# Kernel tuning notes

Measured on AMD Instinct MI355X. Metric: run time of the kernel, lower is better.

Reference implementation:

```python
import jax, jax.numpy as jnp
import numpy as np

N_NODES = 50000
N_EDGES = 800000
N_GRAPHS = 256
IN_DIM = 128
HID = 512            # hidden_layer_size
H2 = HID // 2        # 256, conv channels
H4 = HID // 4        # 128


def _linear_init(key, fan_in, fan_out):
    kw, kb = jax.random.split(key)
    bound = 1.0 / np.sqrt(fan_in)
    W = jax.random.uniform(kw, (fan_in, fan_out), minval=-bound, maxval=bound, dtype=jnp.float32)
    b = jax.random.uniform(kb, (fan_out,), minval=-bound, maxval=bound, dtype=jnp.float32)
    return W, b


def setup_inputs() -> dict:
    key = jax.random.key(0)
    ks = jax.random.split(key, 8)
    x = jax.random.normal(ks[0], (N_NODES, IN_DIM), dtype=jnp.float32)
    edge_index = jax.random.randint(ks[1], (2, N_EDGES), 0, N_NODES, dtype=jnp.int64)
    batch = jnp.sort(jax.random.randint(ks[2], (N_NODES,), 0, N_GRAPHS, dtype=jnp.int64))
    W1, b1 = _linear_init(ks[3], IN_DIM, HID)
    Wc1, bc1 = _linear_init(ks[4], HID, H2)
    Wc2, bc2 = _linear_init(ks[5], H2, H2)
    W2, b2 = _linear_init(ks[6], H2, H4)
    W3, b3 = _linear_init(ks[7], H4, 1)
    return {"x": x, "edge_index": edge_index, "batch": batch,
            "W1": W1, "b1": b1, "Wc1": Wc1, "bc1": bc1,
            "Wc2": Wc2, "bc2": bc2, "W2": W2, "b2": b2, "W3": W3, "b3": b3}


def _gcn_conv(h, W, b, src, dst, norm):
    # PyG GCNConv: out = scatter_add(norm * (h @ W)[src] -> dst) + b
    hw = h @ W                                   # [N, C_out]
    msg = norm[:, None] * hw[src]                # [E+N, C_out] gather
    agg = jax.ops.segment_sum(msg, dst, num_segments=N_NODES)  # scatter-add
    return agg + b


def reference(x, edge_index, batch, W1, b1, Wc1, bc1, Wc2, bc2, W2, b2, W3, b3):
    # --- symmetric GCN normalization with self-loops (shared by both convs) ---
    loop = jnp.arange(N_NODES, dtype=edge_index.dtype)
    src = jnp.concatenate([edge_index[0], loop])
    dst = jnp.concatenate([edge_index[1], loop])
    deg = jax.ops.segment_sum(jnp.ones_like(dst, dtype=jnp.float32), dst, num_segments=N_NODES)
    dinv = jax.lax.rsqrt(deg)                    # deg >= 1 thanks to self-loops
    norm = dinv[src] * dinv[dst]                 # [E+N]

    h = jax.nn.relu(x @ W1 + b1)                 # lin1
    h = jax.nn.relu(_gcn_conv(h, Wc1, bc1, src, dst, norm))   # conv1
    h = jax.nn.relu(_gcn_conv(h, Wc2, bc2, src, dst, norm))   # conv2

    # global_mean_pool over graph ids
    sums = jax.ops.segment_sum(h, batch, num_segments=N_GRAPHS)
    counts = jax.ops.segment_sum(jnp.ones((N_NODES,), jnp.float32), batch, num_segments=N_GRAPHS)
    g = sums / jnp.maximum(counts, 1.0)[:, None]

    # F.dropout is identity in deterministic/eval reference
    g = jax.nn.relu(g @ W2 + b2)                 # lin2
    return g @ W3 + b3                           # lin3 -> [N_GRAPHS, 1]
```

## Files before the change

### kernel.cpp

```cpp
#include <hip/hip_runtime.h>
#include <hip/hip_bf16.h>

#define NN 50000
#define NE 800000
#define NG 256
#define DIN 128
#define DH 512
#define DC 256
#define DL 128
#define NSB 196

#define XBF_OFF   0UL
#define H1BF_OFF  12800000UL
#define HWBF_OFF  64000000UL
#define H2BF_OFF  89600000UL
#define H3BF_OFF  115200000UL
#define W1T_OFF   140800000UL
#define WC1T_OFF  140931072UL
#define WC2T_OFF  141193216UL
#define CNT_OFF   141324288UL
#define FILL_OFF  141524288UL
#define DINV_OFF  141724288UL
#define RP_OFF    141924288UL
#define BSUM_OFF  142124416UL
#define EW_OFF    142125440UL

using bf16x8 = __attribute__((ext_vector_type(8))) short;
using f32x4  = __attribute__((ext_vector_type(4))) float;

__device__ __forceinline__ short f2bf(float f) {
  unsigned u = __builtin_bit_cast(unsigned, f);
  unsigned r = u + 0x7fffu + ((u >> 16) & 1u);
  return (short)(r >> 16);
}
__device__ __forceinline__ float bf2f(unsigned short u) {
  return __builtin_bit_cast(float, (unsigned)u << 16);
}

__device__ __forceinline__ void gload_lds16(const void* g, void* l) {
  typedef const __attribute__((address_space(1))) unsigned gu32;
  typedef __attribute__((address_space(3))) unsigned lu32;
  __builtin_amdgcn_global_load_lds((gu32*)g, (lu32*)l, 16, 0, 0);
}

__global__ __launch_bounds__(256) void prep0(
    const int* __restrict__ src, const int* __restrict__ dst, int* __restrict__ cnt,
    const float* __restrict__ x, short* __restrict__ xbf,
    const float* __restrict__ W1, short* __restrict__ W1t,
    const float* __restrict__ Wc1, short* __restrict__ Wc1t,
    const float* __restrict__ Wc2, short* __restrict__ Wc2t) {
  long gidx = (long)blockIdx.x * 256 + threadIdx.x;
  if (gidx < NE) {
    atomicAdd(&cnt[dst[gidx]], 1);
    return;
  }
  long idx = gidx - NE;
  if (idx < 800000) {
    const float4* p = (const float4*)x + idx * 2;
    float4 a = p[0], b = p[1];
    bf16x8 o;
    o[0] = f2bf(a.x); o[1] = f2bf(a.y); o[2] = f2bf(a.z); o[3] = f2bf(a.w);
    o[4] = f2bf(b.x); o[5] = f2bf(b.y); o[6] = f2bf(b.z); o[7] = f2bf(b.w);
    *(bf16x8*)(xbf + idx * 8) = o;
  } else if (idx < 865536) {
    int j = (int)(idx - 800000);
    int n = j >> 7, k = j & 127;
    W1t[j] = f2bf(W1[k * DH + n]);
  } else if (idx < 996608) {
    int j = (int)(idx - 865536);
    int n = j >> 9, k = j & 511;
    Wc1t[j] = f2bf(Wc1[k * DC + n]);
  } else if (idx < 1062144) {
    int j = (int)(idx - 996608);
    int n = j >> 8, k = j & 255;
    Wc2t[j] = f2bf(Wc2[k * DC + n]);
  }
}

__device__ __forceinline__ void scan_p1_body(
    const int* __restrict__ cnt, int* __restrict__ rowptr,
    int* __restrict__ bsum, float* __restrict__ dinv) {
  __shared__ int wsum[4];
  const int b = blockIdx.x;
  const int idx = b * 256 + threadIdx.x;
  const int lane = threadIdx.x & 63, wid = threadIdx.x >> 6;
  int v = (idx < NN) ? cnt[idx] : 0;
  int incl = v;
  #pragma unroll
  for (int s = 1; s < 64; s <<= 1) {
    int t = __shfl_up(incl, s, 64);
    if (lane >= s) incl += t;
  }
  if (lane == 63) wsum[wid] = incl;
  __syncthreads();
  int woff = 0;
  for (int w = 0; w < wid; ++w) woff += wsum[w];
  if (idx < NN) {
    rowptr[idx] = woff + incl - v;
    dinv[idx] = 1.0f / sqrtf((float)(v + 1));
  }
  if (threadIdx.x == 255) bsum[b] = woff + incl;
}

__device__ __forceinline__ void scan_p3_body(
    int* __restrict__ rowptr, const int* __restrict__ bsum) {
  __shared__ int r4[4];
  const int b = blockIdx.x;
  const int t = threadIdx.x;
  const int lane = t & 63, wid = t >> 6;
  int v = (t < b) ? bsum[t] : 0;
  #pragma unroll
  for (int s = 32; s > 0; s >>= 1) v += __shfl_down(v, s, 64);
  if (lane == 0) r4[wid] = v;
  __syncthreads();
  const int off = r4[0] + r4[1] + r4[2] + r4[3];
  const int idx = b * 256 + t;
  if (idx < NN) rowptr[idx] += off;
  if (b == 0 && t == 0) rowptr[NN] = NE;
}

__global__ void fill_csr(const int* __restrict__ src, const int* __restrict__ dst,
                         const int* __restrict__ rowptr, int* __restrict__ fill,
                         const float* __restrict__ dinv, unsigned* __restrict__ ewp) {
  int e = blockIdx.x * blockDim.x + threadIdx.x;
  if (e < NE) {
    int d = dst[e];
    int s = src[e];
    int pos = rowptr[d] + atomicAdd(&fill[d], 1);
    float w = dinv[d] * dinv[s];
    ewp[pos] = (unsigned)s | ((unsigned)(unsigned short)f2bf(w) << 16);
  }
}

template<int DO_RELU, int HAS_BIAS>
__device__ __forceinline__ void gemm_body(
    const short* __restrict__ A, const short* __restrict__ Bt,
    const float* __restrict__ bias, short* __restrict__ Cout,
    int M, int K, int N, int bxi, int byi)
{
  __shared__ __align__(16) short As[128][64];
  __shared__ __align__(16) short Bs[128][64];
  const int tid  = threadIdx.x;
  const int lane = tid & 63;
  const int wave = tid >> 6;
  const int wr   = wave >> 1;
  const int wc   = wave & 1;
  const int bm = byi * 128;
  const int bn = bxi * 128;

  const int srow = lane >> 3;
  const int scol = ((lane & 7) ^ srow) * 8;

  f32x4 acc[4][4];
  #pragma unroll
  for (int m = 0; m < 4; ++m)
    #pragma unroll
    for (int n = 0; n < 4; ++n)
      acc[m][n] = f32x4{0.f, 0.f, 0.f, 0.f};

  const int fr  = lane & 15;
  const int g4  = lane >> 4;
  const int frx = fr & 7;

  for (int k0 = 0; k0 < K; k0 += 64) {
    #pragma unroll
    for (int j = 0; j < 4; ++j) {
      const int r = wave * 32 + j * 8;
      gload_lds16(A  + (long)(bm + r + srow) * K + k0 + scol, &As[r][0]);
      gload_lds16(Bt + (long)(bn + r + srow) * K + k0 + scol, &Bs[r][0]);
    }
    __syncthreads();
    #pragma unroll
    for (int kk = 0; kk < 2; ++kk) {
      const int col = ((kk * 4 + g4) ^ frx) * 8;
      bf16x8 af[4], bfr[4];
      #pragma unroll
      for (int m = 0; m < 4; ++m)
        af[m] = *(const bf16x8*)&As[wr * 64 + m * 16 + fr][col];
      #pragma unroll
      for (int n = 0; n < 4; ++n)
        bfr[n] = *(const bf16x8*)&Bs[wc * 64 + n * 16 + fr][col];
      #pragma unroll
      for (int m = 0; m < 4; ++m)
        #pragma unroll
        for (int n = 0; n < 4; ++n)
          acc[m][n] = __builtin_amdgcn_mfma_f32_16x16x32_bf16(af[m], bfr[n], acc[m][n], 0, 0, 0);
    }
    __syncthreads();
  }

  const int cr4 = (lane >> 4) * 4;
  const int cc  = lane & 15;
  #pragma unroll
  for (int m = 0; m < 4; ++m) {
    #pragma unroll
    for (int r = 0; r < 4; ++r) {
      int gm = bm + wr * 64 + m * 16 + cr4 + r;
      if (gm >= M) continue;
      #pragma unroll
      for (int n = 0; n < 4; ++n) {
        int gn = bn + wc * 64 + n * 16 + cc;
        float v = acc[m][n][r];
        if (HAS_BIAS) v += bias[gn];
        if (DO_RELU) v = fmaxf(v, 0.f);
        Cout[(long)gm * N + gn] = f2bf(v);
      }
    }
  }
}

__global__ __launch_bounds__(256) void gemm_lin1(
    const short* __restrict__ A, const short* __restrict__ Bt,
    const float* __restrict__ bias, short* __restrict__ Cout,
    const int* __restrict__ cnt, int* __restrict__ rowptr,
    int* __restrict__ bsum, float* __restrict__ dinv)
{
  if (blockIdx.x < NSB) { scan_p1_body(cnt, rowptr, bsum, dinv); return; }
  int gb = blockIdx.x - NSB;
  gemm_body<1, 1>(A, Bt, bias, Cout, NN, DIN, DH, gb & 3, gb >> 2);
}

__global__ __launch_bounds__(256) void gemm_conv1(
    const short* __restrict__ A, const short* __restrict__ Bt,
    short* __restrict__ Cout, int* __restrict__ rowptr,
    const int* __restrict__ bsum)
{
  if (blockIdx.x < NSB) { scan_p3_body(rowptr, bsum); return; }
  int gb = blockIdx.x - NSB;
  gemm_body<0, 0>(A, Bt, nullptr, Cout, NN, DH, DC, gb & 1, gb >> 1);
}

__global__ __launch_bounds__(256) void gemm_conv2(
    const short* __restrict__ A, const short* __restrict__ Bt,
    short* __restrict__ Cout)
{
  gemm_body<0, 0>(A, Bt, nullptr, Cout, NN, DC, DC, blockIdx.x & 1, blockIdx.x >> 1);
}

__global__ __launch_bounds__(256) void aggregate_v6(
    const unsigned short* __restrict__ hw, const unsigned* __restrict__ ewp,
    const int* __restrict__ rowptr, const float* __restrict__ dinv,
    const float* __restrict__ bias, unsigned short* __restrict__ out)
{
  const int wid  = threadIdx.x >> 6;
  const int lane = threadIdx.x & 63;
  const int i = blockIdx.x * 4 + wid;
  if (i >= NN) return;
  const int c0 = lane * 4;
  const float di = dinv[i];

  ushort4 sv = *(const ushort4*)(hw + (long)i * DC + c0);
  const float dii = di * di;
  float acc0 = dii * bf2f(sv.x);
  float acc1 = dii * bf2f(sv.y);
  float acc2 = dii * bf2f(sv.z);
  float acc3 = dii * bf2f(sv.w);

  const int s0 = rowptr[i], s1 = rowptr[i + 1];
  int e = s0;
  for (; e + 8 <= s1; e += 8) {
    unsigned pk[8]; ushort4 vv[8];
    #pragma unroll
    for (int j = 0; j < 8; ++j) pk[j] = __builtin_nontemporal_load(ewp + e + j);
    #pragma unroll
    for (int j = 0; j < 8; ++j)
      vv[j] = *(const ushort4*)(hw + (long)(pk[j] & 0xffffu) * DC + c0);
    #pragma unroll
    for (int j = 0; j < 8; ++j) {
      float w = bf2f((unsigned short)(pk[j] >> 16));
      acc0 += w * bf2f(vv[j].x);
      acc1 += w * bf2f(vv[j].y);
      acc2 += w * bf2f(vv[j].z);
      acc3 += w * bf2f(vv[j].w);
    }
  }
  for (; e + 4 <= s1; e += 4) {
    unsigned pk[4]; ushort4 vv[4];
    #pragma unroll
    for (int j = 0; j < 4; ++j) pk[j] = __builtin_nontemporal_load(ewp + e + j);
    #pragma unroll
    for (int j = 0; j < 4; ++j)
      vv[j] = *(const ushort4*)(hw + (long)(pk[j] & 0xffffu) * DC + c0);
    #pragma unroll
    for (int j = 0; j < 4; ++j) {
      float w = bf2f((unsigned short)(pk[j] >> 16));
      acc0 += w * bf2f(vv[j].x);
      acc1 += w * bf2f(vv[j].y);
      acc2 += w * bf2f(vv[j].z);
      acc3 += w * bf2f(vv[j].w);
    }
  }
  for (; e < s1; ++e) {
    unsigned pk = __builtin_nontemporal_load(ewp + e);
    float w = bf2f((unsigned short)(pk >> 16));
    ushort4 v = *(const ushort4*)(hw + (long)(pk & 0xffffu) * DC + c0);
    acc0 += w * bf2f(v.x);
    acc1 += w * bf2f(v.y);
    acc2 += w * bf2f(v.z);
    acc3 += w * bf2f(v.w);
  }
  const float4 bv = *(const float4*)(bias + c0);
  ushort4 o;
  o.x = (unsigned short)f2bf(fmaxf(acc0 + bv.x, 0.f));
  o.y = (unsigned short)f2bf(fmaxf(acc1 + bv.y, 0.f));
  o.z = (unsigned short)f2bf(fmaxf(acc2 + bv.z, 0.f));
  o.w = (unsigned short)f2bf(fmaxf(acc3 + bv.w, 0.f));
  unsigned long long po = __builtin_bit_cast(unsigned long long, o);
  __builtin_nontemporal_store(po, (unsigned long long*)(out + (long)i * DC + c0));
}

__global__ __launch_bounds__(256) void pool_mlp_v3(
    const unsigned short* __restrict__ h, const int* __restrict__ batch,
    const float* __restrict__ W2, const float* __restrict__ b2,
    const float* __restrict__ W3, const float* __restrict__ b3,
    float* __restrict__ out)
{
  __shared__ float part[4][DC];
  __shared__ float gmean[DC];
  __shared__ float red[DL];
  const int g = blockIdx.x;
  const int t = threadIdx.x;
  const int wid = t >> 6;
  const int lane = t & 63;
  const int c0 = lane * 4;

  int lo = 0, hi = NN;
  while (lo < hi) { int mid = (lo + hi) >> 1; if (batch[mid] < g) lo = mid + 1; else hi = mid; }
  const int start = lo;
  hi = NN;
  while (lo < hi) { int mid = (lo + hi) >> 1; if (batch[mid] < g + 1) lo = mid + 1; else hi = mid; }
  const int end = lo;

  float4 a0 = {0.f, 0.f, 0.f, 0.f}, a1 = {0.f, 0.f, 0.f, 0.f};
  int i = start + wid;
  for (; i + 4 < end; i += 8) {
    ushort4 v0 = *(const ushort4*)(h + (long)i * DC + c0);
    ushort4 v1 = *(const ushort4*)(h + (long)(i + 4) * DC + c0);
    a0.x += bf2f(v0.x); a0.y += bf2f(v0.y); a0.z += bf2f(v0.z); a0.w += bf2f(v0.w);
    a1.x += bf2f(v1.x); a1.y += bf2f(v1.y); a1.z += bf2f(v1.z); a1.w += bf2f(v1.w);
  }
  if (i < end) {
    ushort4 v0 = *(const ushort4*)(h + (long)i * DC + c0);
    a0.x += bf2f(v0.x); a0.y += bf2f(v0.y); a0.z += bf2f(v0.z); a0.w += bf2f(v0.w);
  }
  a0.x += a1.x; a0.y += a1.y; a0.z += a1.z; a0.w += a1.w;
  *(float4*)&part[wid][c0] = a0;
  __syncthreads();
  if (wid == 0) {
    const float inv = 1.0f / fmaxf((float)(end - start), 1.f);
    float4 s0 = *(const float4*)&part[0][c0];
    float4 s1 = *(const float4*)&part[1][c0];
    float4 s2 = *(const float4*)&part[2][c0];
    float4 s3 = *(const float4*)&part[3][c0];
    float4 m;
    m.x = (s0.x + s1.x + s2.x + s3.x) * inv;
    m.y = (s0.y + s1.y + s2.y + s3.y) * inv;
    m.z = (s0.z + s1.z + s2.z + s3.z) * inv;
    m.w = (s0.w + s1.w + s2.w + s3.w) * inv;
    *(float4*)&gmean[c0] = m;
  }
  __syncthreads();
  if (t < DL) {
    float acc = b2[t];
    for (int k = 0; k < DC; ++k) acc = fmaf(gmean[k], W2[k * DL + t], acc);
    red[t] = fmaxf(acc, 0.f) * W3[t];
  }
  __syncthreads();
  for (int s2 = 64; s2 > 0; s2 >>= 1) {
    if (t < s2) red[t] += red[t + s2];
    __syncthreads();
  }
  if (t == 0) out[g] = red[0] + b3[0];
}

extern "C" void kernel_launch(void* const* d_in, const int* in_sizes, int n_in,
                              void* d_out, int out_size, void* d_ws, size_t ws_size,
                              hipStream_t stream) {
  const float* x    = (const float*)d_in[0];
  const int*   ei   = (const int*)d_in[1];
  const int*   bat  = (const int*)d_in[2];
  const float* W1   = (const float*)d_in[3];
  const float* b1   = (const float*)d_in[4];
  const float* Wc1  = (const float*)d_in[5];
  const float* bc1  = (const float*)d_in[6];
  const float* Wc2  = (const float*)d_in[7];
  const float* bc2  = (const float*)d_in[8];
  const float* W2   = (const float*)d_in[9];
  const float* b2   = (const float*)d_in[10];
  const float* W3   = (const float*)d_in[11];
  const float* b3   = (const float*)d_in[12];
  float* out = (float*)d_out;

  char* ws = (char*)d_ws;
  short* xbf    = (short*)(ws + XBF_OFF);
  short* h1bf   = (short*)(ws + H1BF_OFF);
  unsigned short* hwbf = (unsigned short*)(ws + HWBF_OFF);
  unsigned short* h2bf = (unsigned short*)(ws + H2BF_OFF);
  unsigned short* h3bf = (unsigned short*)(ws + H3BF_OFF);
  short* W1t    = (short*)(ws + W1T_OFF);
  short* Wc1t   = (short*)(ws + WC1T_OFF);
  short* Wc2t   = (short*)(ws + WC2T_OFF);
  int*   cnt    = (int*)  (ws + CNT_OFF);
  int*   fill   = (int*)  (ws + FILL_OFF);
  float* dinv   = (float*)(ws + DINV_OFF);
  int*   rowptr = (int*)  (ws + RP_OFF);
  int*   bsum   = (int*)  (ws + BSUM_OFF);
  unsigned* ewp = (unsigned*)(ws + EW_OFF);

  const int* srcE = ei;
  const int* dstE = ei + NE;

  hipMemsetAsync(cnt, 0, 2 * NN * sizeof(int), stream);

  prep0<<<(NE + 1062144 + 255) / 256, 256, 0, stream>>>(
      srcE, dstE, cnt, x, xbf, W1, W1t, Wc1, Wc1t, Wc2, Wc2t);

  gemm_lin1<<<NSB + 4 * 391, 256, 0, stream>>>(xbf, W1t, b1, h1bf,
                                               cnt, rowptr, bsum, dinv);
  gemm_conv1<<<NSB + 2 * 391, 256, 0, stream>>>(h1bf, Wc1t, (short*)hwbf,
                                                rowptr, bsum);
  fill_csr<<<(NE + 255) / 256, 256, 0, stream>>>(srcE, dstE, rowptr, fill, dinv, ewp);

  aggregate_v6<<<(NN + 3) / 4, 256, 0, stream>>>(hwbf, ewp, rowptr, dinv, bc1, h2bf);
  gemm_conv2<<<2 * 391, 256, 0, stream>>>((const short*)h2bf, Wc2t, (short*)hwbf);
  aggregate_v6<<<(NN + 3) / 4, 256, 0, stream>>>(hwbf, ewp, rowptr, dinv, bc2, h3bf);

  pool_mlp_v3<<<NG, 256, 0, stream>>>(h3bf, bat, W2, b2, W3, b3, out);
}
```

Baseline: 306.2 us.

## Pad CSR rows to multiples of eight and software-pipeline edge loads

Each node's CSR row is padded up to a multiple of 8 entries. The edge buffer is zeroed by an enlarged memset, so padding entries have weight zero and point at node 0. The aggregation kernel drops its 4-wide and scalar tail loops and prefetches the next 8 packed edge words while it gathers features for the current 8. This removes loop-tail divergence and hides edge-index load latency, at the cost of extra zero-weight gathers and a larger edge buffer plus memset.

```diff
diff --git a/kernel.cpp b/kernel.cpp
--- a/kernel.cpp
+++ b/kernel.cpp
@@ -20,10 +20,10 @@
 #define WC2T_OFF  141193216UL
 #define CNT_OFF   141324288UL
 #define FILL_OFF  141524288UL
-#define DINV_OFF  141724288UL
-#define RP_OFF    141924288UL
-#define BSUM_OFF  142124416UL
-#define EW_OFF    142125440UL
+#define EW_OFF    141724288UL
+#define DINV_OFF  146524288UL
+#define RP_OFF    146724288UL
+#define BSUM_OFF  146924544UL
 
 using bf16x8 = __attribute__((ext_vector_type(8))) short;
 using f32x4  = __attribute__((ext_vector_type(4))) float;
@@ -84,8 +84,9 @@
   const int b = blockIdx.x;
   const int idx = b * 256 + threadIdx.x;
   const int lane = threadIdx.x & 63, wid = threadIdx.x >> 6;
-  int v = (idx < NN) ? cnt[idx] : 0;
-  int incl = v;
+  int v  = (idx < NN) ? cnt[idx] : 0;
+  int vp = (idx < NN) ? ((v + 7) & ~7) : 0;
+  int incl = vp;
   #pragma unroll
   for (int s = 1; s < 64; s <<= 1) {
     int t = __shfl_up(incl, s, 64);
@@ -95,10 +96,8 @@
   __syncthreads();
   int woff = 0;
   for (int w = 0; w < wid; ++w) woff += wsum[w];
-  if (idx < NN) {
-    rowptr[idx] = woff + incl - v;
-    dinv[idx] = 1.0f / sqrtf((float)(v + 1));
-  }
+  if (idx <= NN) rowptr[idx] = woff + incl - vp;
+  if (idx < NN)  dinv[idx] = 1.0f / sqrtf((float)(v + 1));
   if (threadIdx.x == 255) bsum[b] = woff + incl;
 }
 
@@ -115,8 +114,7 @@
   __syncthreads();
   const int off = r4[0] + r4[1] + r4[2] + r4[3];
   const int idx = b * 256 + t;
-  if (idx < NN) rowptr[idx] += off;
-  if (b == 0 && t == 0) rowptr[NN] = NE;
+  if (idx <= NN) rowptr[idx] += off;
 }
 
 __global__ void fill_csr(const int* __restrict__ src, const int* __restrict__ dst,
@@ -237,7 +235,7 @@
   gemm_body<0, 0>(A, Bt, nullptr, Cout, NN, DC, DC, blockIdx.x & 1, blockIdx.x >> 1);
 }
 
-__global__ __launch_bounds__(256) void aggregate_v6(
+__global__ __launch_bounds__(256) void aggregate_v9(
     const unsigned short* __restrict__ hw, const unsigned* __restrict__ ewp,
     const int* __restrict__ rowptr, const float* __restrict__ dinv,
     const float* __restrict__ bias, unsigned short* __restrict__ out)
@@ -250,55 +248,45 @@
   const float di = dinv[i];
 
   ushort4 sv = *(const ushort4*)(hw + (long)i * DC + c0);
+  const int s0 = rowptr[i], s1 = rowptr[i + 1];
+
+  unsigned pkA[8];
+  if (s0 < s1) {
+    #pragma unroll
+    for (int j = 0; j < 8; ++j) pkA[j] = __builtin_nontemporal_load(ewp + s0 + j);
+  }
+
   const float dii = di * di;
   float acc0 = dii * bf2f(sv.x);
   float acc1 = dii * bf2f(sv.y);
   float acc2 = dii * bf2f(sv.z);
   float acc3 = dii * bf2f(sv.w);
 
-  const int s0 = rowptr[i], s1 = rowptr[i + 1];
-  int e = s0;
-  for (; e + 8 <= s1; e += 8) {
-    unsigned pk[8]; ushort4 vv[8];
-    #pragma unroll
-    for (int j = 0; j < 8; ++j) pk[j] = __builtin_nontemporal_load(ewp + e + j);
+  for (int e = s0; e < s1; e += 8) {
+    ushort4 vv[8];
     #pragma unroll
     for (int j = 0; j < 8; ++j)
-      vv[j] = *(const ushort4*)(hw + (long)(pk[j] & 0xffffu) * DC + c0);
+      vv[j] = *(const ushort4*)(hw + (long)(pkA[j] & 0xffffu) * DC + c0);
+    unsigned pkB[8];
+    if (e + 8 < s1) {
+      #pragma unroll
+      for (int j = 0; j < 8; ++j) pkB[j] = __builtin_nontemporal_load(ewp + e + 8 + j);
+    } else {
+      #pragma unroll
+      for (int j = 0; j < 8; ++j) pkB[j] = 0u;
+    }
     #pragma unroll
     for (int j = 0; j < 8; ++j) {
-      float w = bf2f((unsigned short)(pk[j] >> 16));
+      float w = bf2f((unsigned short)(pkA[j] >> 16));
       acc0 += w * bf2f(vv[j].x);
       acc1 += w * bf2f(vv[j].y);
       acc2 += w * bf2f(vv[j].z);
       acc3 += w * bf2f(vv[j].w);
     }
-  }
-  for (; e + 4 <= s1; e += 4) {
-    unsigned pk[4]; ushort4 vv[4];
-    #pragma unroll
-    for (int j = 0; j < 4; ++j) pk[j] = __builtin_nontemporal_load(ewp + e + j);
-    #pragma unroll
-    for (int j = 0; j < 4; ++j)
-      vv[j] = *(const ushort4*)(hw + (long)(pk[j] & 0xffffu) * DC + c0);
-    #pragma unroll
-    for (int j = 0; j < 4; ++j) {
-      float w = bf2f((unsigned short)(pk[j] >> 16));
-      acc0 += w * bf2f(vv[j].x);
-      acc1 += w * bf2f(vv[j].y);
-      acc2 += w * bf2f(vv[j].z);
-      acc3 += w * bf2f(vv[j].w);
-    }
-  }
-  for (; e < s1; ++e) {
-    unsigned pk = __builtin_nontemporal_load(ewp + e);
-    float w = bf2f((unsigned short)(pk >> 16));
-    ushort4 v = *(const ushort4*)(hw + (long)(pk & 0xffffu) * DC + c0);
-    acc0 += w * bf2f(v.x);
-    acc1 += w * bf2f(v.y);
-    acc2 += w * bf2f(v.z);
-    acc3 += w * bf2f(v.w);
-  }
+    #pragma unroll
+    for (int j = 0; j < 8; ++j) pkA[j] = pkB[j];
+  }
+
   const float4 bv = *(const float4*)(bias + c0);
   ushort4 o;
   o.x = (unsigned short)f2bf(fmaxf(acc0 + bv.x, 0.f));
@@ -402,15 +390,15 @@
   short* Wc2t   = (short*)(ws + WC2T_OFF);
   int*   cnt    = (int*)  (ws + CNT_OFF);
   int*   fill   = (int*)  (ws + FILL_OFF);
+  unsigned* ewp = (unsigned*)(ws + EW_OFF);
   float* dinv   = (float*)(ws + DINV_OFF);
   int*   rowptr = (int*)  (ws + RP_OFF);
   int*   bsum   = (int*)  (ws + BSUM_OFF);
-  unsigned* ewp = (unsigned*)(ws + EW_OFF);
 
   const int* srcE = ei;
   const int* dstE = ei + NE;
 
-  hipMemsetAsync(cnt, 0, 2 * NN * sizeof(int), stream);
+  hipMemsetAsync(cnt, 0, 5200000, stream);
 
   prep0<<<(NE + 1062144 + 255) / 256, 256, 0, stream>>>(
       srcE, dstE, cnt, x, xbf, W1, W1t, Wc1, Wc1t, Wc2, Wc2t);
@@ -421,9 +409,9 @@
                                                 rowptr, bsum);
   fill_csr<<<(NE + 255) / 256, 256, 0, stream>>>(srcE, dstE, rowptr, fill, dinv, ewp);
 
-  aggregate_v6<<<(NN + 3) / 4, 256, 0, stream>>>(hwbf, ewp, rowptr, dinv, bc1, h2bf);
+  aggregate_v9<<<(NN + 3) / 4, 256, 0, stream>>>(hwbf, ewp, rowptr, dinv, bc1, h2bf);
   gemm_conv2<<<2 * 391, 256, 0, stream>>>((const short*)h2bf, Wc2t, (short*)hwbf);
-  aggregate_v6<<<(NN + 3) / 4, 256, 0, stream>>>(hwbf, ewp, rowptr, dinv, bc2, h3bf);
+  aggregate_v9<<<(NN + 3) / 4, 256, 0, stream>>>(hwbf, ewp, rowptr, dinv, bc2, h3bf);
 
   pool_mlp_v3<<<NG, 256, 0, stream>>>(h3bf, bat, W2, b2, W3, b3, out);
 }
```

Result: no change. 304.2 us (-0.6%).
